# Kernel optimization log

Hardware: AMD Instinct MI355X
Metric: run time of the kernel (lower is better)

## Reference

```python
import jax, jax.numpy as jnp
import numpy as np

# SMPL kinematic tree (24 joints)
PARENTS = [-1, 0, 0, 0, 1, 2, 3, 4, 5, 6, 7, 8, 9, 9, 9, 12, 13, 14, 16, 17, 18, 19, 20, 21]
B, V, J, NB = 1024, 6890, 24, 10
POSE_BASIS = 9 * (J - 1)  # 207


def setup_inputs() -> dict:
    key = jax.random.key(0)
    ks = jax.random.split(key, 8)
    betas = jax.random.normal(ks[0], (B, NB), jnp.float32)
    global_rot = jax.random.normal(ks[1], (B, 1, 3, 3), jnp.float32)
    body_pose = jax.random.normal(ks[2], (B, J - 1, 3, 3), jnp.float32)
    v_template = jax.random.normal(ks[3], (V, 3), jnp.float32)
    shapedirs = jax.random.normal(ks[4], (V, 3, NB), jnp.float32) * 0.01
    posedirs = jax.random.normal(ks[5], (POSE_BASIS, V * 3), jnp.float32) * 0.01
    J_regressor = jax.random.uniform(ks[6], (J, V), jnp.float32) / V
    w = jax.random.uniform(ks[7], (V, J), jnp.float32)
    lbs_weights = w / w.sum(-1, keepdims=True)
    return dict(betas=betas, global_rot=global_rot, body_pose=body_pose,
                v_template=v_template, shapedirs=shapedirs, posedirs=posedirs,
                J_regressor=J_regressor, lbs_weights=lbs_weights)


def reference(betas, global_rot, body_pose, v_template, shapedirs, posedirs,
              J_regressor, lbs_weights):
    b = betas.shape[0]
    full_pose = jnp.concatenate([global_rot, body_pose], axis=1)  # [B,24,3,3]

    # shape blend shapes
    v_shaped = v_template + jnp.einsum('bl,vcl->bvc', betas, shapedirs)  # [B,V,3]
    Jt = jnp.einsum('jv,bvc->bjc', J_regressor, v_shaped)  # [B,24,3]

    # pose blend shapes (pose2rot=False: rotations given)
    eye3 = jnp.eye(3, dtype=betas.dtype)
    pose_feature = (full_pose[:, 1:] - eye3).reshape(b, POSE_BASIS)  # [B,207]
    v_posed = v_shaped + (pose_feature @ posedirs).reshape(b, V, 3)

    # forward kinematics along parent chain
    rel_joints = jnp.concatenate(
        [Jt[:, :1], Jt[:, 1:] - Jt[:, jnp.array(PARENTS[1:])]], axis=1)  # [B,24,3]
    top = jnp.concatenate([full_pose, rel_joints[..., None]], axis=-1)  # [B,24,3,4]
    bottom = jnp.broadcast_to(jnp.array([0., 0., 0., 1.], dtype=betas.dtype),
                              (b, J, 1, 4))
    T_local = jnp.concatenate([top, bottom], axis=-2)  # [B,24,4,4]

    chain = [T_local[:, 0]]
    for i in range(1, J):  # fixed small tree, sequential dependency
        chain.append(chain[PARENTS[i]] @ T_local[:, i])
    A = jnp.stack(chain, axis=1)  # [B,24,4,4]

    posed_joints = A[..., :3, 3]  # [B,24,3]
    # make transforms relative to rest-pose joints
    rel_t = posed_joints - jnp.einsum('bjmn,bjn->bjm', A[..., :3, :3], Jt)
    A_rel = A.at[..., :3, 3].set(rel_t)

    # linear blend skinning
    T = jnp.einsum('vj,bjmn->bvmn', lbs_weights, A_rel)  # [B,V,4,4]
    vertices = jnp.einsum('bvmn,bvn->bvm', T[..., :3, :3], v_posed) + T[..., :3, 3]
    return vertices, posed_joints
```

## Files before the change

kernel.cpp:

```cpp
#include <hip/hip_runtime.h>

#define BN 1024
#define NV 6890
#define NBETA 10
#define PB 207
#define N3 20670
#define NCOL 20736
#define NCHUNK 7
#define BT 32

typedef __bf16 bf16x8 __attribute__((ext_vector_type(8)));
typedef float  f32x4  __attribute__((ext_vector_type(4)));

__device__ __constant__ int c_par[24] = {-1,0,0,0,1,2,3,4,5,6,7,8,9,9,9,12,13,14,16,17,18,19,20,21};

__device__ inline unsigned short f2bf(float f) {
    unsigned u = __float_as_uint(f);
    u += 0x7fff + ((u >> 16) & 1);
    return (unsigned short)(u >> 16);
}

__device__ inline void dma16(const void* g, void* l) {
    __builtin_amdgcn_global_load_lds(
        (const __attribute__((address_space(1))) unsigned int*)g,
        (__attribute__((address_space(3))) unsigned int*)l, 16, 0, 0);
}

__global__ __launch_bounds__(256) void k_prep(const float* __restrict__ pd,
                                              const float* __restrict__ sd,
                                              const float* __restrict__ vtm,
                                              const float* __restrict__ Jr,
                                              const float* __restrict__ bpose,
                                              const float* __restrict__ betas,
                                              const float* __restrict__ w,
                                              unsigned short* __restrict__ ws_pdt,
                                              unsigned short* __restrict__ ws_pfb,
                                              unsigned short* __restrict__ ws_wb,
                                              float* __restrict__ ws_jsp)
{
    int blk = blockIdx.x;
    if (blk < 567) {
        int t = blk * 256 + threadIdx.x;
        int kc = t / NCOL;
        int col = t - kc * NCOL;
        bool cok = col < N3;
        unsigned short vals[40];
        #pragma unroll
        for (int kk = 0; kk < 32; kk++) {
            int gk = kc * 32 + kk;
            float val = 0.f;
            if (cok) {
                if (gk < PB)             val = pd[(size_t)gk * N3 + col];
                else if (gk < PB + 10)   val = sd[(size_t)col * NBETA + (gk - PB)];
                else if (gk == PB + 10)  val = vtm[col];
            }
            vals[kk] = f2bf(val);
        }
        #pragma unroll
        for (int kk = 32; kk < 40; kk++) vals[kk] = 0;
        uint4* dst = (uint4*)(ws_pdt + (size_t)t * 40);
        #pragma unroll
        for (int q = 0; q < 5; q++) {
            uint4 u;
            u.x = vals[q*8+0] | ((unsigned)vals[q*8+1] << 16);
            u.y = vals[q*8+2] | ((unsigned)vals[q*8+3] << 16);
            u.z = vals[q*8+4] | ((unsigned)vals[q*8+5] << 16);
            u.w = vals[q*8+6] | ((unsigned)vals[q*8+7] << 16);
            dst[q] = u;
        }
    } else if (blk < 799) {
        int e0 = (blk - 567) * 1024 + threadIdx.x * 4;
        unsigned short v4[4];
        #pragma unroll
        for (int r = 0; r < 4; r++) {
            int e = e0 + r;
            int b = e / 232, k = e - b * 232;
            float x = 0.f;
            if (k < PB) {
                x = bpose[(size_t)b * PB + k];
                int k9 = k % 9;
                if (k9 == 0 || k9 == 4 || k9 == 8) x -= 1.f;
            } else if (k < PB + 10) {
                x = betas[b * NBETA + (k - PB)];
            } else if (k == PB + 10) {
                x = 1.f;
            }
            v4[r] = f2bf(x);
        }
        uint2 u;
        u.x = v4[0] | ((unsigned)v4[1] << 16);
        u.y = v4[2] | ((unsigned)v4[3] << 16);
        *(uint2*)(ws_pfb + e0) = u;
    } else if (blk < 1069) {
        int e0 = (blk - 799) * 1024 + threadIdx.x * 4;
        unsigned short v4[4];
        #pragma unroll
        for (int r = 0; r < 4; r++) {
            int e = e0 + r;
            int v = e / 40, j = e - v * 40;
            float val = (j < 24 && v < NV) ? w[(size_t)v * 24 + j] : 0.f;
            v4[r] = f2bf(val);
        }
        uint2 u;
        u.x = v4[0] | ((unsigned)v4[1] << 16);
        u.y = v4[2] | ((unsigned)v4[3] << 16);
        *(uint2*)(ws_wb + e0) = u;
    } else {
        int b2 = blk - 1069;
        int jc = b2 >> 3;
        int seg = b2 & 7;
        int j = jc / 3, c = jc % 3;
        int v0 = seg * 862;
        int v1 = v0 + 862; if (v1 > NV) v1 = NV;

        float acc[11];
        #pragma unroll
        for (int l = 0; l < 11; l++) acc[l] = 0.f;

        for (int v = v0 + threadIdx.x; v < v1; v += 256) {
            float r = Jr[j * NV + v];
            acc[10] += r * vtm[v * 3 + c];
            const float* s = sd + (size_t)(v * 3 + c) * NBETA;
            #pragma unroll
            for (int l = 0; l < NBETA; l++) acc[l] += r * s[l];
        }

        __shared__ float red[4][11];
        int lane = threadIdx.x & 63, wv = threadIdx.x >> 6;
        #pragma unroll
        for (int l = 0; l < 11; l++) {
            float x = acc[l];
            x += __shfl_down(x, 32, 64);
            x += __shfl_down(x, 16, 64);
            x += __shfl_down(x, 8, 64);
            x += __shfl_down(x, 4, 64);
            x += __shfl_down(x, 2, 64);
            x += __shfl_down(x, 1, 64);
            if (lane == 0) red[wv][l] = x;
        }
        __syncthreads();
        if (threadIdx.x == 0) {
            #pragma unroll
            for (int l = 0; l < 11; l++)
                ws_jsp[((size_t)seg * 72 + jc) * 11 + l]
                    = red[0][l] + red[1][l] + red[2][l] + red[3][l];
        }
    }
}

__global__ __launch_bounds__(256) void k_chain(const float* __restrict__ betas,
                                               const float* __restrict__ grot,
                                               const float* __restrict__ bpose,
                                               const float* __restrict__ ws_jsp,
                                               unsigned short* __restrict__ ws_artb,
                                               float* __restrict__ pj)
{
    __shared__ float js_s[72 * 11];
    __shared__ float jt[16][72];
    __shared__ float tl[16][288];
    __shared__ float am[16][288];
    int tid = threadIdx.x;

    for (int e = tid; e < 72 * 11; e += 256) {
        float s = 0.f;
        #pragma unroll
        for (int seg = 0; seg < 8; seg++)
            s += ws_jsp[(size_t)seg * 792 + e];
        js_s[e] = s;
    }
    __syncthreads();

    int lb = tid >> 4;
    int e  = tid & 15;
    int b  = blockIdx.x * 16 + lb;

    for (int idx = e; idx < 72; idx += 16) {
        float acc = js_s[idx * 11 + 10];
        const float* be = betas + b * NBETA;
        #pragma unroll
        for (int l = 0; l < NBETA; l++) acc += be[l] * js_s[idx * 11 + l];
        jt[lb][idx] = acc;
    }
    __syncthreads();

    for (int idx = e; idx < 288; idx += 16) {
        int j = idx / 12, e12 = idx % 12, m = e12 >> 2, n = e12 & 3;
        float val;
        if (n < 3) {
            val = (j == 0) ? grot[(size_t)b * 9 + m * 3 + n]
                           : bpose[((size_t)b * 23 + (j - 1)) * 9 + m * 3 + n];
        } else {
            val = jt[lb][j * 3 + m];
            if (j > 0) val -= jt[lb][c_par[j] * 3 + m];
        }
        tl[lb][idx] = val;
    }
    __syncthreads();

    if (e < 12) am[lb][e] = tl[lb][e];
    for (int i = 1; i < 24; i++) {
        __syncthreads();
        if (e < 12) {
            int p = c_par[i];
            int m = e >> 2, n = e & 3;
            float val = am[lb][p*12 + m*4 + 0] * tl[lb][i*12 + 0 + n]
                      + am[lb][p*12 + m*4 + 1] * tl[lb][i*12 + 4 + n]
                      + am[lb][p*12 + m*4 + 2] * tl[lb][i*12 + 8 + n];
            if (n == 3) val += am[lb][p*12 + m*4 + 3];
            am[lb][i*12 + e] = val;
        }
    }
    __syncthreads();

    for (int idx = e; idx < 72; idx += 16) {
        int j = idx / 3, m = idx % 3;
        pj[(size_t)b * 72 + idx] = am[lb][j*12 + m*4 + 3];
    }
    for (int idx = e; idx < 480; idx += 16) {
        int col = idx / 40, j = idx - col * 40;
        float val = 0.f;
        if (j < 24) {
            int m = col >> 2, n = col & 3;
            if (n < 3) {
                val = am[lb][j*12 + col];
            } else {
                val = am[lb][j*12 + m*4 + 3]
                    - am[lb][j*12 + m*4 + 0] * jt[lb][j*3 + 0]
                    - am[lb][j*12 + m*4 + 1] * jt[lb][j*3 + 1]
                    - am[lb][j*12 + m*4 + 2] * jt[lb][j*3 + 2];
            }
        }
        ws_artb[(size_t)b * 480 + idx] = f2bf(val);
    }
}

__global__ __launch_bounds__(256, 3) void k_vert(const unsigned short* __restrict__ ws_pdt,
                                                 const unsigned short* __restrict__ ws_pfb,
                                                 const unsigned short* __restrict__ ws_wb,
                                                 const unsigned short* __restrict__ ws_artb,
                                                 float* __restrict__ out)
{
    const int bb = blockIdx.x;
    const int vb = blockIdx.y;
    const int tid = threadIdx.x;
    const int wv = tid >> 6;
    const int lane = tid & 63;
    const int r16 = lane & 15;
    const int half8 = (lane >> 4) * 8;

    __shared__ __align__(16) unsigned char smem[52992];
    unsigned short* pdT_l = (unsigned short*)smem;
    float*          disp_l = (float*)smem;
    unsigned short* ArT_l = (unsigned short*)(smem + 25088);
    float*          T_l   = (float*)(smem + 40448);

    {
        const unsigned short* srcA = ws_artb + (size_t)(bb * BT) * 480;
        for (int i = wv; i < 15; i += 4)
            dma16((const char*)srcA + i * 1024 + lane * 16, (char*)ArT_l + i * 1024);
        const unsigned short* srcP = ws_pdt + (size_t)vb * 192 * 40;
        for (int i = wv; i < 15; i += 4)
            dma16((const char*)srcP + i * 1024 + lane * 16, (char*)pdT_l + i * 1024);
    }

    const unsigned short* pfbase = ws_pfb + (size_t)(bb * BT) * 232;
    bf16x8 a0 = *(const bf16x8*)(pfbase + r16 * 232 + half8);
    bf16x8 a1 = *(const bf16x8*)(pfbase + (16 + r16) * 232 + half8);

    __syncthreads();

    f32x4 acc[2][3];
    #pragma unroll
    for (int mt = 0; mt < 2; mt++)
        #pragma unroll
        for (int t = 0; t < 3; t++)
            acc[mt][t] = (f32x4){0.f, 0.f, 0.f, 0.f};

    #pragma unroll
    for (int kc = 0; kc < NCHUNK; kc++) {
        bf16x8 b0 = *(const bf16x8*)(pdT_l + (wv * 48 + r16) * 40 + half8);
        bf16x8 b1 = *(const bf16x8*)(pdT_l + (wv * 48 + 16 + r16) * 40 + half8);
        bf16x8 b2 = *(const bf16x8*)(pdT_l + (wv * 48 + 32 + r16) * 40 + half8);
        bf16x8 a0n, a1n;
        if (kc < NCHUNK - 1) {
            a0n = *(const bf16x8*)(pfbase + r16 * 232 + (kc + 1) * 32 + half8);
            a1n = *(const bf16x8*)(pfbase + (16 + r16) * 232 + (kc + 1) * 32 + half8);
        }
        __syncthreads();
        if (kc < NCHUNK - 1) {
            const unsigned short* src = ws_pdt + ((size_t)(kc + 1) * NCOL + (size_t)vb * 192) * 40;
            for (int i = wv; i < 15; i += 4)
                dma16((const char*)src + i * 1024 + lane * 16, (char*)pdT_l + i * 1024);
        }
        acc[0][0] = __builtin_amdgcn_mfma_f32_16x16x32_bf16(a0, b0, acc[0][0], 0, 0, 0);
        acc[1][0] = __builtin_amdgcn_mfma_f32_16x16x32_bf16(a1, b0, acc[1][0], 0, 0, 0);
        acc[0][1] = __builtin_amdgcn_mfma_f32_16x16x32_bf16(a0, b1, acc[0][1], 0, 0, 0);
        acc[1][1] = __builtin_amdgcn_mfma_f32_16x16x32_bf16(a1, b1, acc[1][1], 0, 0, 0);
        acc[0][2] = __builtin_amdgcn_mfma_f32_16x16x32_bf16(a0, b2, acc[0][2], 0, 0, 0);
        acc[1][2] = __builtin_amdgcn_mfma_f32_16x16x32_bf16(a1, b2, acc[1][2], 0, 0, 0);
        a0 = a0n; a1 = a1n;
        if (kc < NCHUNK - 1) __syncthreads();
    }

    #pragma unroll
    for (int mt = 0; mt < 2; mt++) {
        #pragma unroll
        for (int t = 0; t < 3; t++) {
            int col = wv * 48 + t * 16 + r16;
            int brow = mt * 16 + (lane >> 4) * 4;
            #pragma unroll
            for (int r = 0; r < 4; r++)
                disp_l[(brow + r) * 196 + col] = acc[mt][t][r];
        }
    }
    __syncthreads();

    bf16x8 aw = *(const bf16x8*)(ws_wb + (size_t)(vb * 64 + wv * 16 + r16) * 40 + half8);

    const int vg = vb * 64 + lane;

    for (int half = 0; half < 2; half++) {
        if (half == 1) {
            const unsigned short* srcA = ws_artb + (size_t)(bb * BT + 16) * 480;
            for (int i = wv; i < 15; i += 4)
                dma16((const char*)srcA + i * 1024 + lane * 16, (char*)ArT_l + i * 1024);
            __syncthreads();
        }
        for (int s = 0; s < 4; s++) {
            int sub = half * 4 + s;
            bf16x8 bA0 = *(const bf16x8*)(ArT_l + (s * 48 + r16) * 40 + half8);
            bf16x8 bA1 = *(const bf16x8*)(ArT_l + (s * 48 + 16 + r16) * 40 + half8);
            bf16x8 bA2 = *(const bf16x8*)(ArT_l + (s * 48 + 32 + r16) * 40 + half8);
            f32x4 z = (f32x4){0.f, 0.f, 0.f, 0.f};
            f32x4 t0 = __builtin_amdgcn_mfma_f32_16x16x32_bf16(aw, bA0, z, 0, 0, 0);
            f32x4 t1 = __builtin_amdgcn_mfma_f32_16x16x32_bf16(aw, bA1, z, 0, 0, 0);
            f32x4 t2 = __builtin_amdgcn_mfma_f32_16x16x32_bf16(aw, bA2, z, 0, 0, 0);

            int vrow = wv * 16 + (lane >> 4) * 4;
            #pragma unroll
            for (int r = 0; r < 4; r++) {
                T_l[(vrow + r) * 49 + r16]      = t0[r];
                T_l[(vrow + r) * 49 + 16 + r16] = t1[r];
                T_l[(vrow + r) * 49 + 32 + r16] = t2[r];
            }
            __syncthreads();

            if (vg < NV) {
                const float* Tv = &T_l[lane * 49 + wv * 12];
                float x = disp_l[(sub * 4 + wv) * 196 + lane * 3 + 0];
                float y = disp_l[(sub * 4 + wv) * 196 + lane * 3 + 1];
                float zz = disp_l[(sub * 4 + wv) * 196 + lane * 3 + 2];
                size_t b = (size_t)(bb * BT + sub * 4 + wv);
                float* o = out + b * N3 + (size_t)vg * 3;
                o[0] = Tv[0] * x + Tv[1] * y + Tv[2]  * zz + Tv[3];
                o[1] = Tv[4] * x + Tv[5] * y + Tv[6]  * zz + Tv[7];
                o[2] = Tv[8] * x + Tv[9] * y + Tv[10] * zz + Tv[11];
            }
            __syncthreads();
        }
    }
}

extern "C" void kernel_launch(void* const* d_in, const int* in_sizes, int n_in,
                              void* d_out, int out_size, void* d_ws, size_t ws_size,
                              hipStream_t stream) {
    const float* betas = (const float*)d_in[0];
    const float* grot  = (const float*)d_in[1];
    const float* bpose = (const float*)d_in[2];
    const float* vtm   = (const float*)d_in[3];
    const float* sd    = (const float*)d_in[4];
    const float* pd    = (const float*)d_in[5];
    const float* Jr    = (const float*)d_in[6];
    const float* w     = (const float*)d_in[7];
    float* out = (float*)d_out;

    char* ws = (char*)d_ws;
    unsigned short* ws_pdt  = (unsigned short*)(ws);
    unsigned short* ws_pfb  = (unsigned short*)(ws + 11612160);
    unsigned short* ws_wb   = (unsigned short*)(ws + 12087296);
    float*          ws_jsp  = (float*)         (ws + 12640256);
    unsigned short* ws_artb = (unsigned short*)(ws + 12665600);

    k_prep<<<1645, 256, 0, stream>>>(pd, sd, vtm, Jr, bpose, betas, w,
                                     ws_pdt, ws_pfb, ws_wb, ws_jsp);
    k_chain<<<BN / 16, 256, 0, stream>>>(betas, grot, bpose, ws_jsp, ws_artb,
                                         out + (size_t)BN * N3);
    k_vert<<<dim3(32, 108), 256, 0, stream>>>(ws_pdt, ws_pfb, ws_wb, ws_artb, out);
}
```

Measured before the change: 188.1 us.

## Restructure vertex kernel: K-contiguous posedirs, direct loads, DPP skinning, staged stores

The bf16 posedirs workspace is re-laid out so each column's K values are contiguous (stride 224). The pose-blend GEMM now reads its B operand straight from global memory instead of through LDS async copies with per-chunk barriers. Skinning no longer writes the blended transform matrix to LDS. It multiplies MFMA outputs by displaced vertex coordinates and reduces across quads with DPP, then stages results in a double-buffered LDS tile for coalesced output stores. The joint-regression prep blocks are merged so each block handles all three coordinates of one joint. This trades LDS traffic and barriers for more global/L2 reads of posedirs, since each batch-tile block re-fetches them.

```diff
diff --git a/kernel.cpp b/kernel.cpp
--- a/kernel.cpp
+++ b/kernel.cpp
@@ -20,10 +20,11 @@
     return (unsigned short)(u >> 16);
 }
 
-__device__ inline void dma16(const void* g, void* l) {
-    __builtin_amdgcn_global_load_lds(
-        (const __attribute__((address_space(1))) unsigned int*)g,
-        (__attribute__((address_space(3))) unsigned int*)l, 16, 0, 0);
+__device__ inline float quad_reduce_add(float x) {
+    int a = __builtin_amdgcn_update_dpp(0, __float_as_int(x), 0xB1, 0xF, 0xF, true);
+    float x2 = x + __int_as_float(a);
+    int b = __builtin_amdgcn_update_dpp(0, __float_as_int(x2), 0x4E, 0xF, 0xF, true);
+    return x2 + __int_as_float(b);
 }
 
 __global__ __launch_bounds__(256) void k_prep(const float* __restrict__ pd,
@@ -40,11 +41,10 @@
 {
     int blk = blockIdx.x;
     if (blk < 567) {
-        int t = blk * 256 + threadIdx.x;
-        int kc = t / NCOL;
-        int col = t - kc * NCOL;
+        int kc = blk / 81;
+        int col = (blk - kc * 81) * 256 + threadIdx.x;
         bool cok = col < N3;
-        unsigned short vals[40];
+        unsigned short vals[32];
         #pragma unroll
         for (int kk = 0; kk < 32; kk++) {
             int gk = kc * 32 + kk;
@@ -56,11 +56,9 @@
             }
             vals[kk] = f2bf(val);
         }
-        #pragma unroll
-        for (int kk = 32; kk < 40; kk++) vals[kk] = 0;
-        uint4* dst = (uint4*)(ws_pdt + (size_t)t * 40);
-        #pragma unroll
-        for (int q = 0; q < 5; q++) {
+        uint4* dst = (uint4*)(ws_pdt + (size_t)col * 224 + kc * 32);
+        #pragma unroll
+        for (int q = 0; q < 4; q++) {
             uint4 u;
             u.x = vals[q*8+0] | ((unsigned)vals[q*8+1] << 16);
             u.y = vals[q*8+2] | ((unsigned)vals[q*8+3] << 16);
@@ -107,28 +105,31 @@
         *(uint2*)(ws_wb + e0) = u;
     } else {
         int b2 = blk - 1069;
-        int jc = b2 >> 3;
+        int j = b2 >> 3;
         int seg = b2 & 7;
-        int j = jc / 3, c = jc % 3;
         int v0 = seg * 862;
         int v1 = v0 + 862; if (v1 > NV) v1 = NV;
 
-        float acc[11];
-        #pragma unroll
-        for (int l = 0; l < 11; l++) acc[l] = 0.f;
+        float acc[33];
+        #pragma unroll
+        for (int l = 0; l < 33; l++) acc[l] = 0.f;
 
         for (int v = v0 + threadIdx.x; v < v1; v += 256) {
             float r = Jr[j * NV + v];
-            acc[10] += r * vtm[v * 3 + c];
-            const float* s = sd + (size_t)(v * 3 + c) * NBETA;
+            const float* s = sd + (size_t)v * 30;
             #pragma unroll
-            for (int l = 0; l < NBETA; l++) acc[l] += r * s[l];
-        }
-
-        __shared__ float red[4][11];
+            for (int c = 0; c < 3; c++) {
+                #pragma unroll
+                for (int l = 0; l < NBETA; l++)
+                    acc[c * 11 + l] += r * s[c * 10 + l];
+                acc[c * 11 + 10] += r * vtm[v * 3 + c];
+            }
+        }
+
+        __shared__ float red[4][33];
         int lane = threadIdx.x & 63, wv = threadIdx.x >> 6;
         #pragma unroll
-        for (int l = 0; l < 11; l++) {
+        for (int l = 0; l < 33; l++) {
             float x = acc[l];
             x += __shfl_down(x, 32, 64);
             x += __shfl_down(x, 16, 64);
@@ -139,12 +140,10 @@
             if (lane == 0) red[wv][l] = x;
         }
         __syncthreads();
-        if (threadIdx.x == 0) {
-            #pragma unroll
-            for (int l = 0; l < 11; l++)
-                ws_jsp[((size_t)seg * 72 + jc) * 11 + l]
-                    = red[0][l] + red[1][l] + red[2][l] + red[3][l];
-        }
+        if (threadIdx.x < 33)
+            ws_jsp[(size_t)seg * 792 + j * 33 + threadIdx.x] =
+                red[0][threadIdx.x] + red[1][threadIdx.x] +
+                red[2][threadIdx.x] + red[3][threadIdx.x];
     }
 }
 
@@ -246,28 +245,14 @@
     const int wv = tid >> 6;
     const int lane = tid & 63;
     const int r16 = lane & 15;
-    const int half8 = (lane >> 4) * 8;
-
-    __shared__ __align__(16) unsigned char smem[52992];
-    unsigned short* pdT_l = (unsigned short*)smem;
-    float*          disp_l = (float*)smem;
-    unsigned short* ArT_l = (unsigned short*)(smem + 25088);
-    float*          T_l   = (float*)(smem + 40448);
-
-    {
-        const unsigned short* srcA = ws_artb + (size_t)(bb * BT) * 480;
-        for (int i = wv; i < 15; i += 4)
-            dma16((const char*)srcA + i * 1024 + lane * 16, (char*)ArT_l + i * 1024);
-        const unsigned short* srcP = ws_pdt + (size_t)vb * 192 * 40;
-        for (int i = wv; i < 15; i += 4)
-            dma16((const char*)srcP + i * 1024 + lane * 16, (char*)pdT_l + i * 1024);
-    }
+    const int quad = lane >> 4;
+    const int half8 = quad * 8;
+
+    __shared__ float disp3[10432];
+    __shared__ float out_l[2][4 * 196];
 
     const unsigned short* pfbase = ws_pfb + (size_t)(bb * BT) * 232;
-    bf16x8 a0 = *(const bf16x8*)(pfbase + r16 * 232 + half8);
-    bf16x8 a1 = *(const bf16x8*)(pfbase + (16 + r16) * 232 + half8);
-
-    __syncthreads();
+    const unsigned short* pdbase = ws_pdt + (size_t)(vb * 192 + wv * 48) * 224;
 
     f32x4 acc[2][3];
     #pragma unroll
@@ -278,28 +263,17 @@
 
     #pragma unroll
     for (int kc = 0; kc < NCHUNK; kc++) {
-        bf16x8 b0 = *(const bf16x8*)(pdT_l + (wv * 48 + r16) * 40 + half8);
-        bf16x8 b1 = *(const bf16x8*)(pdT_l + (wv * 48 + 16 + r16) * 40 + half8);
-        bf16x8 b2 = *(const bf16x8*)(pdT_l + (wv * 48 + 32 + r16) * 40 + half8);
-        bf16x8 a0n, a1n;
-        if (kc < NCHUNK - 1) {
-            a0n = *(const bf16x8*)(pfbase + r16 * 232 + (kc + 1) * 32 + half8);
-            a1n = *(const bf16x8*)(pfbase + (16 + r16) * 232 + (kc + 1) * 32 + half8);
-        }
-        __syncthreads();
-        if (kc < NCHUNK - 1) {
-            const unsigned short* src = ws_pdt + ((size_t)(kc + 1) * NCOL + (size_t)vb * 192) * 40;
-            for (int i = wv; i < 15; i += 4)
-                dma16((const char*)src + i * 1024 + lane * 16, (char*)pdT_l + i * 1024);
-        }
+        bf16x8 a0 = *(const bf16x8*)(pfbase + r16 * 232 + kc * 32 + half8);
+        bf16x8 a1 = *(const bf16x8*)(pfbase + (16 + r16) * 232 + kc * 32 + half8);
+        bf16x8 b0 = *(const bf16x8*)(pdbase + (size_t)r16 * 224 + kc * 32 + half8);
+        bf16x8 b1 = *(const bf16x8*)(pdbase + (size_t)(16 + r16) * 224 + kc * 32 + half8);
+        bf16x8 b2 = *(const bf16x8*)(pdbase + (size_t)(32 + r16) * 224 + kc * 32 + half8);
         acc[0][0] = __builtin_amdgcn_mfma_f32_16x16x32_bf16(a0, b0, acc[0][0], 0, 0, 0);
         acc[1][0] = __builtin_amdgcn_mfma_f32_16x16x32_bf16(a1, b0, acc[1][0], 0, 0, 0);
         acc[0][1] = __builtin_amdgcn_mfma_f32_16x16x32_bf16(a0, b1, acc[0][1], 0, 0, 0);
         acc[1][1] = __builtin_amdgcn_mfma_f32_16x16x32_bf16(a1, b1, acc[1][1], 0, 0, 0);
         acc[0][2] = __builtin_amdgcn_mfma_f32_16x16x32_bf16(a0, b2, acc[0][2], 0, 0, 0);
         acc[1][2] = __builtin_amdgcn_mfma_f32_16x16x32_bf16(a1, b2, acc[1][2], 0, 0, 0);
-        a0 = a0n; a1 = a1n;
-        if (kc < NCHUNK - 1) __syncthreads();
     }
 
     #pragma unroll
@@ -307,56 +281,65 @@
         #pragma unroll
         for (int t = 0; t < 3; t++) {
             int col = wv * 48 + t * 16 + r16;
-            int brow = mt * 16 + (lane >> 4) * 4;
+            int vloc = col / 3, c = col - vloc * 3;
+            int brow = mt * 16 + quad * 4;
             #pragma unroll
             for (int r = 0; r < 4; r++)
-                disp_l[(brow + r) * 196 + col] = acc[mt][t][r];
-        }
+                disp3[vloc * 163 + (brow + r) * 5 + c] = acc[mt][t][r];
+        }
+    }
+    #pragma unroll
+    for (int i = 0; i < 8; i++) {
+        int e = tid + i * 256;
+        int v = e >> 5, b = e & 31;
+        disp3[v * 163 + b * 5 + 3] = 1.f;
     }
     __syncthreads();
 
     bf16x8 aw = *(const bf16x8*)(ws_wb + (size_t)(vb * 64 + wv * 16 + r16) * 40 + half8);
 
-    const int vg = vb * 64 + lane;
-
-    for (int half = 0; half < 2; half++) {
-        if (half == 1) {
-            const unsigned short* srcA = ws_artb + (size_t)(bb * BT + 16) * 480;
-            for (int i = wv; i < 15; i += 4)
-                dma16((const char*)srcA + i * 1024 + lane * 16, (char*)ArT_l + i * 1024);
-            __syncthreads();
-        }
-        for (int s = 0; s < 4; s++) {
-            int sub = half * 4 + s;
-            bf16x8 bA0 = *(const bf16x8*)(ArT_l + (s * 48 + r16) * 40 + half8);
-            bf16x8 bA1 = *(const bf16x8*)(ArT_l + (s * 48 + 16 + r16) * 40 + half8);
-            bf16x8 bA2 = *(const bf16x8*)(ArT_l + (s * 48 + 32 + r16) * 40 + half8);
-            f32x4 z = (f32x4){0.f, 0.f, 0.f, 0.f};
-            f32x4 t0 = __builtin_amdgcn_mfma_f32_16x16x32_bf16(aw, bA0, z, 0, 0, 0);
-            f32x4 t1 = __builtin_amdgcn_mfma_f32_16x16x32_bf16(aw, bA1, z, 0, 0, 0);
-            f32x4 t2 = __builtin_amdgcn_mfma_f32_16x16x32_bf16(aw, bA2, z, 0, 0, 0);
-
-            int vrow = wv * 16 + (lane >> 4) * 4;
-            #pragma unroll
-            for (int r = 0; r < 4; r++) {
-                T_l[(vrow + r) * 49 + r16]      = t0[r];
-                T_l[(vrow + r) * 49 + 16 + r16] = t1[r];
-                T_l[(vrow + r) * 49 + 32 + r16] = t2[r];
-            }
-            __syncthreads();
-
-            if (vg < NV) {
-                const float* Tv = &T_l[lane * 49 + wv * 12];
-                float x = disp_l[(sub * 4 + wv) * 196 + lane * 3 + 0];
-                float y = disp_l[(sub * 4 + wv) * 196 + lane * 3 + 1];
-                float zz = disp_l[(sub * 4 + wv) * 196 + lane * 3 + 2];
-                size_t b = (size_t)(bb * BT + sub * 4 + wv);
-                float* o = out + b * N3 + (size_t)vg * 3;
-                o[0] = Tv[0] * x + Tv[1] * y + Tv[2]  * zz + Tv[3];
-                o[1] = Tv[4] * x + Tv[5] * y + Tv[6]  * zz + Tv[7];
-                o[2] = Tv[8] * x + Tv[9] * y + Tv[10] * zz + Tv[11];
-            }
-            __syncthreads();
+    const int q16 = r16 >> 2;
+    const int sel = r16 & 3;
+    int gsel = sel * 16 + q16 * 4;
+    int bq = gsel / 12;
+    int mq = (gsel - 12 * bq) >> 2;
+    int bl[3], nn[3];
+    #pragma unroll
+    for (int i = 0; i < 3; i++) {
+        int g = i * 16 + r16;
+        bl[i] = g / 12;
+        nn[i] = (g - 12 * bl[i]) & 3;
+    }
+
+    for (int sub = 0; sub < 8; sub++) {
+        const unsigned short* Abase = ws_artb + ((size_t)(bb * BT + sub * 4) * 12) * 40;
+        bf16x8 bA0 = *(const bf16x8*)(Abase + (size_t)r16 * 40 + half8);
+        bf16x8 bA1 = *(const bf16x8*)(Abase + (size_t)(16 + r16) * 40 + half8);
+        bf16x8 bA2 = *(const bf16x8*)(Abase + (size_t)(32 + r16) * 40 + half8);
+        f32x4 z = (f32x4){0.f, 0.f, 0.f, 0.f};
+        f32x4 t0 = __builtin_amdgcn_mfma_f32_16x16x32_bf16(aw, bA0, z, 0, 0, 0);
+        f32x4 t1 = __builtin_amdgcn_mfma_f32_16x16x32_bf16(aw, bA1, z, 0, 0, 0);
+        f32x4 t2 = __builtin_amdgcn_mfma_f32_16x16x32_bf16(aw, bA2, z, 0, 0, 0);
+
+        int buf = sub & 1;
+        #pragma unroll
+        for (int r = 0; r < 4; r++) {
+            int vloc = wv * 16 + quad * 4 + r;
+            int vbase = vloc * 163 + (sub * 4) * 5;
+            float s0 = quad_reduce_add(t0[r] * disp3[vbase + bl[0] * 5 + nn[0]]);
+            float s1 = quad_reduce_add(t1[r] * disp3[vbase + bl[1] * 5 + nn[1]]);
+            float s2 = quad_reduce_add(t2[r] * disp3[vbase + bl[2] * 5 + nn[2]]);
+            float sv = (sel == 0) ? s0 : ((sel == 1) ? s1 : s2);
+            if (sel < 3)
+                out_l[buf][bq * 196 + vloc * 3 + mq] = sv;
+        }
+        __syncthreads();
+
+        for (int e = tid; e < 4 * 192; e += 256) {
+            int b_l = e / 192, idx = e - b_l * 192;
+            int gcol = vb * 192 + idx;
+            if (gcol < N3)
+                out[((size_t)(bb * BT + sub * 4 + b_l)) * N3 + gcol] = out_l[buf][b_l * 196 + idx];
         }
     }
 }
@@ -376,12 +359,12 @@
 
     char* ws = (char*)d_ws;
     unsigned short* ws_pdt  = (unsigned short*)(ws);
-    unsigned short* ws_pfb  = (unsigned short*)(ws + 11612160);
-    unsigned short* ws_wb   = (unsigned short*)(ws + 12087296);
-    float*          ws_jsp  = (float*)         (ws + 12640256);
-    unsigned short* ws_artb = (unsigned short*)(ws + 12665600);
-
-    k_prep<<<1645, 256, 0, stream>>>(pd, sd, vtm, Jr, bpose, betas, w,
+    unsigned short* ws_pfb  = (unsigned short*)(ws + 9289728);
+    unsigned short* ws_wb   = (unsigned short*)(ws + 9764864);
+    float*          ws_jsp  = (float*)         (ws + 10317824);
+    unsigned short* ws_artb = (unsigned short*)(ws + 10343168);
+
+    k_prep<<<1261, 256, 0, stream>>>(pd, sd, vtm, Jr, bpose, betas, w,
                                      ws_pdt, ws_pfb, ws_wb, ws_jsp);
     k_chain<<<BN / 16, 256, 0, stream>>>(betas, grot, bpose, ws_jsp, ws_artb,
                                          out + (size_t)BN * N3);
```

After: 209.9 us. 1.12x slower.
